# Kernel optimization log

Measured on AMD Instinct MI355X. Metric: run time of the kernel, lower is better.

The kernel has to match this reference:

```python
import jax, jax.numpy as jnp
import numpy as np
import hashlib

# Model hyperparameters (from VictorASIFractalLightModel defaults)
B, L, D = 2, 2048, 1024
VOCAB, TOOL_VOCAB = 65536, 128
STEPS = 8            # FractalEmbedding steps -> 2*STEPS = 16 features
N_CONV, N_ATTN = 10, 6
HEADS, Q_GROUPS = 8, 2
HPG = HEADS // Q_GROUPS
HEAD_DIM = D // HEADS
KSIZE = 5
EPS = 1e-5


def _token_to_c(token_ids_np):
    # sha256-based complex constant per token id (exactly as in FractalEmbedding)
    flat = token_ids_np.reshape(-1)
    out = np.empty((flat.size, 2), dtype=np.float32)
    for i, tid in enumerate(flat):
        h = hashlib.sha256(str(int(tid)).encode()).hexdigest()
        out[i, 0] = (int(h[:16], 16) / 2**64 - 0.5) * 2.0
        out[i, 1] = (int(h[16:32], 16) / 2**64 - 0.5) * 2.0
    return out.reshape(token_ids_np.shape + (2,))


def _julia_feats(cs):
    # Vectorized julia iteration, z starts at 0.  cs: [B, L, 2] -> feats [B, L, 2*STEPS]
    cr, ci = cs[..., 0], cs[..., 1]
    zr = jnp.zeros_like(cr)
    zi = jnp.zeros_like(ci)
    feats = []
    for _ in range(STEPS):
        zr, zi = zr * zr - zi * zi + cr, 2.0 * zr * zi + ci
        feats.append(zr)
        feats.append(zi)
    return jnp.stack(feats, axis=-1)


def _layer_norm(x, s, b):
    mu = jnp.mean(x, axis=-1, keepdims=True)
    var = jnp.mean(jnp.square(x - mu), axis=-1, keepdims=True)
    return (x - mu) * jax.lax.rsqrt(var + EPS) * s + b


def _conv_block(x, dw_w, dw_b, pw_w, pw_b, ln_s, ln_b):
    # x: [B, L, D] -> depthwise conv (k=5, same pad) -> pointwise conv to 2D -> GLU -> residual LN
    xc = jnp.transpose(x, (0, 2, 1))  # [B, D, L]
    y = jax.lax.conv_general_dilated(xc, dw_w, (1,), [(KSIZE // 2, KSIZE // 2)],
                                     dimension_numbers=("NCH", "OIH", "NCH"),
                                     feature_group_count=D) + dw_b[None, :, None]
    y = jax.lax.conv_general_dilated(y, pw_w, (1,), [(0, 0)],
                                     dimension_numbers=("NCH", "OIH", "NCH")) + pw_b[None, :, None]
    y = jnp.transpose(y, (0, 2, 1))  # [B, L, 2D]
    a, gate = jnp.split(y, 2, axis=-1)
    return _layer_norm(x + a * jax.nn.sigmoid(gate), ln_s, ln_b)


def _attention(x, qw, kvw, ow, ln_s, ln_b):
    # Grouped-query attention with an explicit (unfused) score tensor, per the source.
    Bx, Lx, Dx = x.shape
    q = (x @ qw).reshape(Bx, Lx, Q_GROUPS, HPG, HEAD_DIM)
    kv = (x @ kvw).reshape(Bx, Lx, HEADS, 2, HEAD_DIM)
    k = kv[..., 0, :].reshape(Bx, Lx, Q_GROUPS, HPG, HEAD_DIM)
    v = kv[..., 1, :].reshape(Bx, Lx, Q_GROUPS, HPG, HEAD_DIM)
    scale = HEAD_DIM ** -0.5
    scores = jnp.einsum("bqghd,bkghd->bghqk", q, k) * scale  # [B, g, hpg, Lq, Lk]
    attn = jax.nn.softmax(scores, axis=-1)
    out = jnp.einsum("bghqk,bkghd->bqghd", attn, v).reshape(Bx, Lx, Dx)
    return _layer_norm(x + out @ ow, ln_s, ln_b)


def setup_inputs() -> dict:
    key = jax.random.key(0)
    ks = jax.random.split(key, 10)
    token_ids = jax.random.randint(ks[0], (B, L), 0, VOCAB)
    cs = jnp.asarray(_token_to_c(np.asarray(token_ids)))
    return {
        "token_ids": token_ids,
        "cs": cs,
        "proj_w": jax.random.normal(ks[1], (2 * STEPS, D), dtype=jnp.float32) * 0.25,
        "emb_scale": jnp.ones((1,), dtype=jnp.float32),
        "conv_dw_w": jax.random.normal(ks[2], (N_CONV, D, 1, KSIZE), dtype=jnp.float32) * 0.2,
        "conv_dw_b": jnp.zeros((N_CONV, D), dtype=jnp.float32),
        "conv_pw_w": jax.random.normal(ks[3], (N_CONV, 2 * D, D, 1), dtype=jnp.float32) * (D ** -0.5),
        "conv_pw_b": jnp.zeros((N_CONV, 2 * D), dtype=jnp.float32),
        "conv_ln_s": jnp.ones((N_CONV, D), dtype=jnp.float32),
        "conv_ln_b": jnp.zeros((N_CONV, D), dtype=jnp.float32),
        "attn_q_w": jax.random.normal(ks[4], (N_ATTN, D, D), dtype=jnp.float32) * (D ** -0.5),
        "attn_kv_w": jax.random.normal(ks[5], (N_ATTN, D, 2 * D), dtype=jnp.float32) * (D ** -0.5),
        "attn_out_w": jax.random.normal(ks[6], (N_ATTN, D, D), dtype=jnp.float32) * (D ** -0.5),
        "attn_ln_s": jnp.ones((N_ATTN, D), dtype=jnp.float32),
        "attn_ln_b": jnp.zeros((N_ATTN, D), dtype=jnp.float32),
        "lm_w": jax.random.normal(ks[7], (D, VOCAB), dtype=jnp.float32) * (D ** -0.5),
        "tool_w": jax.random.normal(ks[8], (D, TOOL_VOCAB), dtype=jnp.float32) * (D ** -0.5),
        "tool_b": jnp.zeros((TOOL_VOCAB,), dtype=jnp.float32),
    }


def reference(token_ids, cs, proj_w, emb_scale, conv_dw_w, conv_dw_b, conv_pw_w, conv_pw_b,
              conv_ln_s, conv_ln_b, attn_q_w, attn_kv_w, attn_out_w, attn_ln_s, attn_ln_b,
              lm_w, tool_w, tool_b):
    feats = _julia_feats(cs)                 # [B, L, 16]
    h = (feats @ proj_w) * emb_scale         # FractalEmbedding
    for i in range(N_CONV):
        h = _conv_block(h, conv_dw_w[i], conv_dw_b[i], conv_pw_w[i], conv_pw_b[i],
                        conv_ln_s[i], conv_ln_b[i])
    for i in range(N_ATTN):
        h = _attention(h, attn_q_w[i], attn_kv_w[i], attn_out_w[i], attn_ln_s[i], attn_ln_b[i])
    # ReplayMemoryStack is a side-effecting identity on h.
    last = h[:, -1, :]
    gen_logits = last @ lm_w
    tool_logits = last @ tool_w + tool_b
    return gen_logits, tool_logits
```

## Files before the change

### kernel.cpp

```cpp
#include <hip/hip_runtime.h>
#include <hip/hip_bf16.h>
#include <math.h>

#define B_ 2
#define L_ 2048
#define D_ 1024
#define VOCAB_ 65536
#define TOOLV_ 128
#define NCONV_ 10
#define NATTN_ 6
#define HEADS_ 8
#define HD_ 128
#define EPS_ 1e-5f

typedef short bf16x8 __attribute__((ext_vector_type(8)));
typedef short short4v __attribute__((ext_vector_type(4)));
typedef float f32x4 __attribute__((ext_vector_type(4)));
#define MFMA16(a,b,c) __builtin_amdgcn_mfma_f32_16x16x32_bf16(a, b, c, 0, 0, 0)

__device__ inline short f2bf(float f) {
  __hip_bfloat16 h = __float2bfloat16(f);
  return *reinterpret_cast<short*>(&h);
}

__device__ __forceinline__ void gld16(const void* g, void* l) {
  __builtin_amdgcn_global_load_lds(
      (const __attribute__((address_space(1))) unsigned int*)g,
      (__attribute__((address_space(3))) unsigned int*)l, 16, 0, 0);
}

__device__ __forceinline__ void sync_prefetch() {
  asm volatile("s_waitcnt vmcnt(0)" ::: "memory");
  __builtin_amdgcn_s_barrier();
  __builtin_amdgcn_sched_barrier(0);
}

__global__ __launch_bounds__(256) void julia_proj_k(const float* __restrict__ cs,
    const float* __restrict__ pw, const float* __restrict__ esc, float* __restrict__ h) {
  int row = blockIdx.x;
  float cr = cs[2*(size_t)row], ci = cs[2*(size_t)row+1];
  float f[16];
  float zr = 0.f, zi = 0.f;
  #pragma unroll
  for (int s = 0; s < 8; ++s) {
    float nzr = zr*zr - zi*zi + cr;
    float nzi = 2.f*zr*zi + ci;
    zr = nzr; zi = nzi;
    f[2*s] = zr; f[2*s+1] = zi;
  }
  float e = esc[0];
  int d = threadIdx.x * 4;
  float4 acc = {0.f, 0.f, 0.f, 0.f};
  #pragma unroll
  for (int i = 0; i < 16; ++i) {
    float4 pv = *(const float4*)(pw + i*D_ + d);
    acc.x += f[i]*pv.x; acc.y += f[i]*pv.y; acc.z += f[i]*pv.z; acc.w += f[i]*pv.w;
  }
  acc.x *= e; acc.y *= e; acc.z *= e; acc.w *= e;
  *(float4*)(h + (size_t)row*D_ + d) = acc;
}

__global__ __launch_bounds__(256) void dwconv_k(const float* __restrict__ x,
    const float* __restrict__ w, const float* __restrict__ bias, short* __restrict__ y) {
  int idx = blockIdx.x*256 + threadIdx.x;
  int d = (idx & (D_/4 - 1)) * 4;
  int bl = idx >> 8;
  int l = bl & (L_-1);
  size_t bbase = (size_t)(bl >> 11) * L_;
  float4 acc = *(const float4*)(bias + d);
  float wr[4][5];
  #pragma unroll
  for (int j = 0; j < 4; ++j)
    #pragma unroll
    for (int k = 0; k < 5; ++k) wr[j][k] = w[(d+j)*5 + k];
  #pragma unroll
  for (int k = 0; k < 5; ++k) {
    int ll = l + k - 2;
    if (ll >= 0 && ll < L_) {
      float4 xv = *(const float4*)(x + (bbase + ll)*D_ + d);
      acc.x += xv.x*wr[0][k]; acc.y += xv.y*wr[1][k];
      acc.z += xv.z*wr[2][k]; acc.w += xv.w*wr[3][k];
    }
  }
  short4v o = { f2bf(acc.x), f2bf(acc.y), f2bf(acc.z), f2bf(acc.w) };
  ((short4v*)y)[idx] = o;
}

__global__ __launch_bounds__(256) void cvt_bf16_k(const float* __restrict__ x,
    short* __restrict__ y, int n4) {
  int i = blockIdx.x*256 + threadIdx.x;
  if (i >= n4) return;
  float4 v = ((const float4*)x)[i];
  short4v s = { f2bf(v.x), f2bf(v.y), f2bf(v.z), f2bf(v.w) };
  ((short4v*)y)[i] = s;
}

__global__ __launch_bounds__(256) void transp_bf16_k(const float* __restrict__ W0,
    short* __restrict__ WT0, int K, int N, size_t srcStride, size_t dstStride) {
  const float* W = W0 + blockIdx.z*srcStride;
  short* WT = WT0 + blockIdx.z*dstStride;
  __shared__ short t[32][33];
  int n0 = blockIdx.x*32, k0 = blockIdx.y*32;
  int tx = threadIdx.x & 31, ty = threadIdx.x >> 5;
  #pragma unroll
  for (int i = 0; i < 4; ++i) {
    int k = ty + i*8;
    t[tx][k] = f2bf(W[(size_t)(k0+k)*N + n0 + tx]);
  }
  __syncthreads();
  #pragma unroll
  for (int i = 0; i < 4; ++i) {
    int n = ty + i*8;
    WT[(size_t)(n0+n)*K + k0 + tx] = t[n][tx];
  }
}

template<int MODE, bool BIAS>
__global__ __launch_bounds__(256) void gemm_bf16(const short* __restrict__ A,
    const short* __restrict__ Bt, const float* __restrict__ bias,
    float* __restrict__ C, short* __restrict__ obf,
    short* __restrict__ kbf, short* __restrict__ vtbf,
    float scale, int M, int N, int K) {
  __shared__ short As[2][128*32];
  __shared__ short Bs[2][128*32];
  const int tid  = threadIdx.x;
  const int lane = tid & 63;
  const int wave = tid >> 6;
  const int wm = wave >> 1, wn = wave & 1;
  const int g = lane >> 4, c = lane & 15;
  const int m0 = blockIdx.x * 128, n0 = blockIdx.y * 128;

  f32x4 acc[4][4];
  #pragma unroll
  for (int i = 0; i < 4; ++i)
    #pragma unroll
    for (int j = 0; j < 4; ++j) acc[i][j] = (f32x4){0.f,0.f,0.f,0.f};

  const int srow = wave*16 + (lane>>2);
  const int scol = (lane&3)*8;
  const short* aSrc0 = A + (size_t)(m0 + srow)*K + scol;
  const short* aSrc1 = aSrc0 + (size_t)64*K;
  const short* bSrc0 = Bt + (size_t)(n0 + srow)*K + scol;
  const short* bSrc1 = bSrc0 + (size_t)64*K;
  const int woff = wave*512;

  gld16(aSrc0, &As[0][woff]);
  gld16(aSrc1, &As[0][woff + 2048]);
  gld16(bSrc0, &Bs[0][woff]);
  gld16(bSrc1, &Bs[0][woff + 2048]);
  sync_prefetch();

  const int nt = K >> 5;
  int cur = 0;
  for (int t = 0; t < nt; ++t) {
    if (t + 1 < nt) {
      int k0 = (t + 1) << 5;
      gld16(aSrc0 + k0, &As[cur^1][woff]);
      gld16(aSrc1 + k0, &As[cur^1][woff + 2048]);
      gld16(bSrc0 + k0, &Bs[cur^1][woff]);
      gld16(bSrc1 + k0, &Bs[cur^1][woff + 2048]);
    }
    bf16x8 af[4], bfr[4];
    #pragma unroll
    for (int mi = 0; mi < 4; ++mi)
      af[mi] = *(const bf16x8*)&As[cur][(wm*64 + mi*16 + c)*32 + g*8];
    #pragma unroll
    for (int ni = 0; ni < 4; ++ni)
      bfr[ni] = *(const bf16x8*)&Bs[cur][(wn*64 + ni*16 + c)*32 + g*8];
    #pragma unroll
    for (int mi = 0; mi < 4; ++mi)
      #pragma unroll
      for (int ni = 0; ni < 4; ++ni)
        acc[mi][ni] = MFMA16(af[mi], bfr[ni], acc[mi][ni]);
    if (t + 1 < nt) {
      sync_prefetch();
      cur ^= 1;
    }
  }

  #pragma unroll
  for (int mi = 0; mi < 4; ++mi) {
    int row = m0 + wm*64 + mi*16 + g*4;
    #pragma unroll
    for (int ni = 0; ni < 4; ++ni) {
      int col = n0 + wn*64 + ni*16 + c;
      if (MODE == 0) {
        float bv = BIAS ? bias[col] : 0.f;
        #pragma unroll
        for (int r = 0; r < 4; ++r)
          C[(size_t)(row+r)*N + col] = acc[mi][ni][r] + bv;
      } else {
        if (col < 1024) {
          #pragma unroll
          for (int r = 0; r < 4; ++r)
            obf[(size_t)(row+r)*1024 + col] = f2bf(acc[mi][ni][r]*scale);
        } else {
          int col2 = col - 1024;
          int hh = col2 >> 8, jj = (col2 >> 7) & 1, d = col2 & 127;
          int bb = row >> 11, l = row & 2047;
          size_t bh = (size_t)bb*8 + hh;
          if (jj == 0) {
            #pragma unroll
            for (int r = 0; r < 4; ++r)
              kbf[(bh*L_ + l + r)*128 + d] = f2bf(acc[mi][ni][r]);
          } else {
            #pragma unroll
            for (int r = 0; r < 4; ++r)
              vtbf[(bh*128 + d)*L_ + l + r] = f2bf(acc[mi][ni][r]);
          }
        }
      }
    }
  }
}

__global__ __launch_bounds__(256) void glu_ln_k(float* __restrict__ h,
    const float* __restrict__ y2, const float* __restrict__ s, const float* __restrict__ b,
    short* __restrict__ bo) {
  int row = blockIdx.x;
  int tid = threadIdx.x;
  int d = tid*4;
  float* xr = h + (size_t)row*D_;
  const float* yr = y2 + (size_t)row*2*D_;
  __shared__ float red[256];
  float4 xv = *(const float4*)(xr + d);
  float4 av = *(const float4*)(yr + d);
  float4 gv = *(const float4*)(yr + D_ + d);
  float v[4];
  v[0] = xv.x + av.x/(1.f + expf(-gv.x));
  v[1] = xv.y + av.y/(1.f + expf(-gv.y));
  v[2] = xv.z + av.z/(1.f + expf(-gv.z));
  v[3] = xv.w + av.w/(1.f + expf(-gv.w));
  red[tid] = v[0]+v[1]+v[2]+v[3]; __syncthreads();
  for (int st = 128; st > 0; st >>= 1) { if (tid < st) red[tid] += red[tid+st]; __syncthreads(); }
  float mu = red[0] * (1.f/D_); __syncthreads();
  float lv = 0.f;
  #pragma unroll
  for (int j = 0; j < 4; ++j) { float dd = v[j]-mu; lv += dd*dd; }
  red[tid] = lv; __syncthreads();
  for (int st = 128; st > 0; st >>= 1) { if (tid < st) red[tid] += red[tid+st]; __syncthreads(); }
  float var = red[0] * (1.f/D_);
  float r = 1.f/sqrtf(var + EPS_);
  float4 sv = *(const float4*)(s + d);
  float4 bv = *(const float4*)(b + d);
  float4 o;
  o.x = (v[0]-mu)*r*sv.x + bv.x;
  o.y = (v[1]-mu)*r*sv.y + bv.y;
  o.z = (v[2]-mu)*r*sv.z + bv.z;
  o.w = (v[3]-mu)*r*sv.w + bv.w;
  *(float4*)(xr + d) = o;
  if (bo) {
    short4v ob = { f2bf(o.x), f2bf(o.y), f2bf(o.z), f2bf(o.w) };
    *(short4v*)(bo + (size_t)row*D_ + d) = ob;
  }
}

__global__ __launch_bounds__(256) void resid_ln_k(float* __restrict__ h,
    const float* __restrict__ proj, const float* __restrict__ s, const float* __restrict__ b,
    short* __restrict__ bo) {
  int row = blockIdx.x;
  int tid = threadIdx.x;
  int d = tid*4;
  float* xr = h + (size_t)row*D_;
  const float* pr = proj + (size_t)row*D_;
  __shared__ float red[256];
  float4 xv = *(const float4*)(xr + d);
  float4 pv = *(const float4*)(pr + d);
  float v[4] = { xv.x+pv.x, xv.y+pv.y, xv.z+pv.z, xv.w+pv.w };
  red[tid] = v[0]+v[1]+v[2]+v[3]; __syncthreads();
  for (int st = 128; st > 0; st >>= 1) { if (tid < st) red[tid] += red[tid+st]; __syncthreads(); }
  float mu = red[0] * (1.f/D_); __syncthreads();
  float lv = 0.f;
  #pragma unroll
  for (int j = 0; j < 4; ++j) { float dd = v[j]-mu; lv += dd*dd; }
  red[tid] = lv; __syncthreads();
  for (int st = 128; st > 0; st >>= 1) { if (tid < st) red[tid] += red[tid+st]; __syncthreads(); }
  float var = red[0] * (1.f/D_);
  float r = 1.f/sqrtf(var + EPS_);
  float4 sv = *(const float4*)(s + d);
  float4 bv = *(const float4*)(b + d);
  float4 o;
  o.x = (v[0]-mu)*r*sv.x + bv.x;
  o.y = (v[1]-mu)*r*sv.y + bv.y;
  o.z = (v[2]-mu)*r*sv.z + bv.z;
  o.w = (v[3]-mu)*r*sv.w + bv.w;
  *(float4*)(xr + d) = o;
  if (bo) {
    short4v ob = { f2bf(o.x), f2bf(o.y), f2bf(o.z), f2bf(o.w) };
    *(short4v*)(bo + (size_t)row*D_ + d) = ob;
  }
}

#define PPITCH 72
__global__ __launch_bounds__(256) void attn2_k(const short* __restrict__ qbf,
    const short* __restrict__ kbf, const short* __restrict__ vtbf,
    short* __restrict__ obf) {
  __shared__ short Ks[2][64*128];
  __shared__ short Vts[2][128*64];
  __shared__ short Ps[4*16*PPITCH];

  const int tid  = threadIdx.x;
  const int wave = tid >> 6;
  const int lane = tid & 63;
  const int g    = lane >> 4;
  const int c    = lane & 15;
  const int hh   = blockIdx.y;
  const int b    = blockIdx.z;
  const int q0   = blockIdx.x*64 + wave*16;
  const size_t bh = (size_t)(b*HEADS_ + hh);

  bf16x8 qf[4];
  {
    const short* Qp = qbf + ((size_t)(b*L_ + q0 + c))*D_ + hh*HD_;
    #pragma unroll
    for (int kd = 0; kd < 4; ++kd)
      qf[kd] = *(const bf16x8*)(Qp + kd*32 + g*8);
  }

  f32x4 O[8];
  #pragma unroll
  for (int i = 0; i < 8; ++i) O[i] = (f32x4){0.f,0.f,0.f,0.f};
  float mrun[4] = {-INFINITY,-INFINITY,-INFINITY,-INFINITY};
  float lrun[4] = {0.f,0.f,0.f,0.f};
  short* Pw = Ps + wave*16*PPITCH;

  const short* kBase = kbf + bh*L_*128;
  const short* vBase = vtbf + bh*128*L_;

  auto stage = [&](int t, int buf) {
    #pragma unroll
    for (int rd = 0; rd < 4; ++rd) {
      int slot = rd*256 + tid;
      int kr = slot >> 4, kj = slot & 15;
      int vr = slot >> 3, vj = slot & 7;
      gld16(kBase + ((size_t)(t*64 + kr))*128 + ((kj ^ (kr & 15)) * 8),
            (char*)&Ks[buf][0] + (rd*256 + wave*64)*16);
      gld16(vBase + (size_t)vr*L_ + t*64 + ((vj ^ (vr & 7)) * 8),
            (char*)&Vts[buf][0] + (rd*256 + wave*64)*16);
    }
  };

  stage(0, 0);
  sync_prefetch();
  int cur = 0;
  const int NT = L_/64;

  for (int t = 0; t < NT; ++t) {
    if (t + 1 < NT) stage(t + 1, cur^1);

    f32x4 s[4];
    #pragma unroll
    for (int nc = 0; nc < 4; ++nc) {
      s[nc] = (f32x4){0.f,0.f,0.f,0.f};
      int R = nc*16 + c;
      #pragma unroll
      for (int kd = 0; kd < 4; ++kd) {
        bf16x8 kf = *(const bf16x8*)&Ks[cur][R*128 + (((kd*4 + g) ^ (R & 15)) * 8)];
        s[nc] = MFMA16(qf[kd], kf, s[nc]);
      }
    }

    float tm[4], rsum[4], alpha[4];
    #pragma unroll
    for (int r = 0; r < 4; ++r)
      tm[r] = fmaxf(fmaxf(s[0][r], s[1][r]), fmaxf(s[2][r], s[3][r]));
    #pragma unroll
    for (int r = 0; r < 4; ++r) {
      #pragma unroll
      for (int mask = 1; mask <= 8; mask <<= 1)
        tm[r] = fmaxf(tm[r], __shfl_xor(tm[r], mask));
      float mnew = fmaxf(mrun[r], tm[r]);
      alpha[r] = expf(mrun[r] - mnew);
      mrun[r] = mnew;
      rsum[r] = 0.f;
    }
    #pragma unroll
    for (int nc = 0; nc < 4; ++nc)
      #pragma unroll
      for (int r = 0; r < 4; ++r) {
        float p = expf(s[nc][r] - mrun[r]);
        s[nc][r] = p;
        rsum[r] += p;
      }
    #pragma unroll
    for (int r = 0; r < 4; ++r) {
      #pragma unroll
      for (int mask = 1; mask <= 8; mask <<= 1)
        rsum[r] += __shfl_xor(rsum[r], mask);
      lrun[r] = lrun[r]*alpha[r] + rsum[r];
    }
    #pragma unroll
    for (int nc = 0; nc < 8; ++nc)
      #pragma unroll
      for (int r = 0; r < 4; ++r) O[nc][r] *= alpha[r];

    #pragma unroll
    for (int nc = 0; nc < 4; ++nc)
      #pragma unroll
      for (int r = 0; r < 4; ++r)
        Pw[(g*4+r)*PPITCH + nc*16 + c] = f2bf(s[nc][r]);
    asm volatile("s_waitcnt lgkmcnt(0)" ::: "memory");
    bf16x8 pa0 = *(const bf16x8*)&Pw[c*PPITCH + g*8];
    bf16x8 pa1 = *(const bf16x8*)&Pw[c*PPITCH + 32 + g*8];

    #pragma unroll
    for (int ks = 0; ks < 2; ++ks) {
      #pragma unroll
      for (int nc = 0; nc < 8; ++nc) {
        int R = nc*16 + c;
        bf16x8 vf = *(const bf16x8*)&Vts[cur][R*64 + (((ks*4 + g) ^ (R & 7)) * 8)];
        O[nc] = MFMA16(ks ? pa1 : pa0, vf, O[nc]);
      }
    }

    if (t + 1 < NT) {
      sync_prefetch();
      cur ^= 1;
    }
  }

  short* ob = obf + ((size_t)(b*L_ + q0))*D_ + hh*HD_;
  #pragma unroll
  for (int r = 0; r < 4; ++r) {
    float inv = 1.f / lrun[r];
    #pragma unroll
    for (int nc = 0; nc < 8; ++nc)
      ob[(size_t)(g*4+r)*D_ + nc*16 + c] = f2bf(O[nc][r] * inv);
  }
}

__global__ __launch_bounds__(256) void lm_head_part_k(const float* __restrict__ h,
    const float* __restrict__ lm_w, float* __restrict__ part) {
  int tid = threadIdx.x;
  int n = (blockIdx.x*256 + tid)*4;
  int ks = blockIdx.y;
  __shared__ float last0[256], last1[256];
  const float* h0 = h + ((size_t)0*L_ + (L_-1))*D_ + ks*256;
  const float* h1 = h + ((size_t)1*L_ + (L_-1))*D_ + ks*256;
  last0[tid] = h0[tid]; last1[tid] = h1[tid];
  __syncthreads();
  float4 a0 = {0.f,0.f,0.f,0.f}, a1 = {0.f,0.f,0.f,0.f};
  const float* wp = lm_w + (size_t)(ks*256)*VOCAB_ + n;
  for (int kk = 0; kk < 256; ++kk) {
    float4 wv = *(const float4*)(wp + (size_t)kk*VOCAB_);
    float c0 = last0[kk], c1 = last1[kk];
    a0.x += c0*wv.x; a0.y += c0*wv.y; a0.z += c0*wv.z; a0.w += c0*wv.w;
    a1.x += c1*wv.x; a1.y += c1*wv.y; a1.z += c1*wv.z; a1.w += c1*wv.w;
  }
  *(float4*)(part + ((size_t)ks*2 + 0)*VOCAB_ + n) = a0;
  *(float4*)(part + ((size_t)ks*2 + 1)*VOCAB_ + n) = a1;
}

__global__ __launch_bounds__(256) void lm_head_red_k(const float* __restrict__ part,
    float* __restrict__ out) {
  int i = blockIdx.x*256 + threadIdx.x;
  int j = (i*4) / VOCAB_;
  int n = (i*4) & (VOCAB_-1);
  float4 acc = {0.f,0.f,0.f,0.f};
  #pragma unroll
  for (int ks = 0; ks < 4; ++ks) {
    float4 v = *(const float4*)(part + ((size_t)ks*2 + j)*VOCAB_ + n);
    acc.x += v.x; acc.y += v.y; acc.z += v.z; acc.w += v.w;
  }
  *(float4*)(out + (size_t)j*VOCAB_ + n) = acc;
}

__global__ __launch_bounds__(128) void tool_head_k(const float* __restrict__ h,
    const float* __restrict__ tw, const float* __restrict__ tb, float* __restrict__ out) {
  int b = blockIdx.x;
  int tid = threadIdx.x;
  __shared__ float last[D_];
  const float* hr = h + ((size_t)b*L_ + (L_-1))*D_;
  for (int d = tid; d < D_; d += 128) last[d] = hr[d];
  __syncthreads();
  float acc = tb[tid];
  for (int k = 0; k < D_; ++k) acc += last[k]*tw[(size_t)k*TOOLV_ + tid];
  out[(size_t)2*VOCAB_ + (size_t)b*TOOLV_ + tid] = acc;
}

extern "C" void kernel_launch(void* const* d_in, const int* in_sizes, int n_in,
                              void* d_out, int out_size, void* d_ws, size_t ws_size,
                              hipStream_t stream) {
  const float* cs        = (const float*)d_in[1];
  const float* proj_w    = (const float*)d_in[2];
  const float* emb_scale = (const float*)d_in[3];
  const float* conv_dw_w = (const float*)d_in[4];
  const float* conv_dw_b = (const float*)d_in[5];
  const float* conv_pw_w = (const float*)d_in[6];
  const float* conv_pw_b = (const float*)d_in[7];
  const float* conv_ln_s = (const float*)d_in[8];
  const float* conv_ln_b = (const float*)d_in[9];
  const float* attn_q_w  = (const float*)d_in[10];
  const float* attn_kv_w = (const float*)d_in[11];
  const float* attn_out_w= (const float*)d_in[12];
  const float* attn_ln_s = (const float*)d_in[13];
  const float* attn_ln_b = (const float*)d_in[14];
  const float* lm_w      = (const float*)d_in[15];
  const float* tool_w    = (const float*)d_in[16];
  const float* tool_b    = (const float*)d_in[17];

  const int M = B_*L_;
  float* h    = (float*)d_ws;
  float* buf2 = h    + (size_t)M*D_;
  short* kbf  = (short*)(buf2 + (size_t)M*2*D_);
  short* vtbf = kbf + (size_t)B_*HEADS_*L_*128;
  short* abf  = (short*)(vtbf + (size_t)B_*HEADS_*128*L_);
  short* wconv= abf + (size_t)M*D_;
  short* wqkv = wconv + (size_t)NCONV_*2*D_*D_;
  short* wout = wqkv + (size_t)NATTN_*3*D_*D_;
  float* lmpart = (float*)(wout + (size_t)NATTN_*D_*D_);
  short* qbf  = (short*)(buf2 + (size_t)M*D_);

  const float scale = 0.088388347648318447f;

  {
    int n4 = NCONV_*2*D_*D_/4;
    cvt_bf16_k<<<(n4 + 255)/256, 256, 0, stream>>>(conv_pw_w, wconv, n4);
    transp_bf16_k<<<dim3(D_/32, D_/32, NATTN_), 256, 0, stream>>>(
        attn_q_w, wqkv, D_, D_, (size_t)D_*D_, (size_t)3*D_*D_);
    transp_bf16_k<<<dim3((2*D_)/32, D_/32, NATTN_), 256, 0, stream>>>(
        attn_kv_w, wqkv + (size_t)D_*D_, D_, 2*D_, (size_t)D_*2*D_, (size_t)3*D_*D_);
    transp_bf16_k<<<dim3(D_/32, D_/32, NATTN_), 256, 0, stream>>>(
        attn_out_w, wout, D_, D_, (size_t)D_*D_, (size_t)D_*D_);
  }

  julia_proj_k<<<M, 256, 0, stream>>>(cs, proj_w, emb_scale, h);

  for (int i = 0; i < NCONV_; ++i) {
    dwconv_k<<<(M*D_/4)/256, 256, 0, stream>>>(h, conv_dw_w + (size_t)i*D_*5,
                                               conv_dw_b + (size_t)i*D_, abf);
    gemm_bf16<0, true><<<dim3(M/128, (2*D_)/128), 256, 0, stream>>>(
        abf, wconv + (size_t)i*2*D_*D_, conv_pw_b + (size_t)i*2*D_,
        buf2, nullptr, nullptr, nullptr, 1.f, M, 2*D_, D_);
    glu_ln_k<<<M, 256, 0, stream>>>(h, buf2, conv_ln_s + (size_t)i*D_,
                                    conv_ln_b + (size_t)i*D_,
                                    (i == NCONV_-1) ? abf : (short*)nullptr);
  }

  for (int i = 0; i < NATTN_; ++i) {
    gemm_bf16<3, false><<<dim3(M/128, (3*D_)/128), 256, 0, stream>>>(
        abf, wqkv + (size_t)i*3*D_*D_, nullptr, nullptr, qbf, kbf, vtbf,
        scale, M, 3*D_, D_);
    attn2_k<<<dim3(L_/64, HEADS_, B_), 256, 0, stream>>>(qbf, kbf, vtbf, abf);
    gemm_bf16<0, false><<<dim3(M/128, D_/128), 256, 0, stream>>>(
        abf, wout + (size_t)i*D_*D_, nullptr, buf2, nullptr, nullptr, nullptr,
        1.f, M, D_, D_);
    resid_ln_k<<<M, 256, 0, stream>>>(h, buf2, attn_ln_s + (size_t)i*D_,
                                      attn_ln_b + (size_t)i*D_,
                                      (i < NATTN_-1) ? abf : (short*)nullptr);
  }

  lm_head_part_k<<<dim3(VOCAB_/1024, 4), 256, 0, stream>>>(h, lm_w, lmpart);
  lm_head_red_k<<<(2*VOCAB_/4)/256, 256, 0, stream>>>(lmpart, (float*)d_out);
  tool_head_k<<<B_, 128, 0, stream>>>(h, tool_w, tool_b, (float*)d_out);
}
```

Before: 1.811 ms.

## Fuse GLU into pointwise GEMM epilogue and swizzle GEMM/attention block order

The conv pointwise weights are row-permuted at setup so that each GEMM tile holds matching 'a' and 'gate' columns. The GEMM epilogue can then apply bias and sigmoid gating and write a single D-wide output, and the LayerNorm reuses the plain residual kernel. This removes writing and re-reading the 2D-wide intermediate. Workgroup IDs in the GEMM and attention kernels are also remapped with a stride-8 swizzle, probably to spread blocks across XCDs and improve L2 locality. The swizzle hardcodes grid sizes (32 M-tiles, a 512-block attention grid), which ties the kernels to these shapes.

```diff
diff --git a/kernel.cpp b/kernel.cpp
--- a/kernel.cpp
+++ b/kernel.cpp
@@ -86,13 +86,19 @@
   ((short4v*)y)[idx] = o;
 }
 
-__global__ __launch_bounds__(256) void cvt_bf16_k(const float* __restrict__ x,
-    short* __restrict__ y, int n4) {
-  int i = blockIdx.x*256 + threadIdx.x;
-  if (i >= n4) return;
-  float4 v = ((const float4*)x)[i];
+__global__ __launch_bounds__(256) void cvt_perm_k(const float* __restrict__ W,
+    short* __restrict__ out) {
+  int z = blockIdx.y;
+  int i4 = blockIdx.x*256 + threadIdx.x;
+  int e = i4*4;
+  int r = e >> 10, k = e & 1023;
+  int t = r >> 7, wn = (r >> 6) & 1, j = r & 63;
+  int u = t*64 + wn*32 + (j & 31);
+  int src = (j < 32) ? u : 1024 + u;
+  const float* p = W + ((size_t)z*2048 + src)*1024 + k;
+  float4 v = *(const float4*)p;
   short4v s = { f2bf(v.x), f2bf(v.y), f2bf(v.z), f2bf(v.w) };
-  ((short4v*)y)[i] = s;
+  *(short4v*)(out + ((size_t)z*2048 + r)*1024 + k) = s;
 }
 
 __global__ __launch_bounds__(256) void transp_bf16_k(const float* __restrict__ W0,
@@ -115,7 +121,7 @@
   }
 }
 
-template<int MODE, bool BIAS>
+template<int MODE>
 __global__ __launch_bounds__(256) void gemm_bf16(const short* __restrict__ A,
     const short* __restrict__ Bt, const float* __restrict__ bias,
     float* __restrict__ C, short* __restrict__ obf,
@@ -128,7 +134,12 @@
   const int wave = tid >> 6;
   const int wm = wave >> 1, wn = wave & 1;
   const int g = lane >> 4, c = lane & 15;
-  const int m0 = blockIdx.x * 128, n0 = blockIdx.y * 128;
+
+  int flat = blockIdx.y * gridDim.x + blockIdx.x;
+  int nwg  = gridDim.x * gridDim.y;
+  int swz  = (flat & 7) * (nwg >> 3) + (flat >> 3);
+  const int m0 = (swz & 31) * 128;
+  const int n0 = (swz >> 5) * 128;
 
   f32x4 acc[4][4];
   #pragma unroll
@@ -178,6 +189,25 @@
     }
   }
 
+  if (MODE == 4) {
+    #pragma unroll
+    for (int mi = 0; mi < 4; ++mi) {
+      int row = m0 + wm*64 + mi*16 + g*4;
+      #pragma unroll
+      for (int ni = 0; ni < 2; ++ni) {
+        int u = (n0 >> 7)*64 + wn*32 + ni*16 + c;
+        float ba = bias[u], bg = bias[1024 + u];
+        #pragma unroll
+        for (int r = 0; r < 4; ++r) {
+          float a  = acc[mi][ni][r]   + ba;
+          float gt = acc[mi][ni+2][r] + bg;
+          C[(size_t)(row+r)*1024 + u] = a / (1.f + expf(-gt));
+        }
+      }
+    }
+    return;
+  }
+
   #pragma unroll
   for (int mi = 0; mi < 4; ++mi) {
     int row = m0 + wm*64 + mi*16 + g*4;
@@ -185,10 +215,9 @@
     for (int ni = 0; ni < 4; ++ni) {
       int col = n0 + wn*64 + ni*16 + c;
       if (MODE == 0) {
-        float bv = BIAS ? bias[col] : 0.f;
         #pragma unroll
         for (int r = 0; r < 4; ++r)
-          C[(size_t)(row+r)*N + col] = acc[mi][ni][r] + bv;
+          C[(size_t)(row+r)*N + col] = acc[mi][ni][r];
       } else {
         if (col < 1024) {
           #pragma unroll
@@ -214,23 +243,18 @@
   }
 }
 
-__global__ __launch_bounds__(256) void glu_ln_k(float* __restrict__ h,
-    const float* __restrict__ y2, const float* __restrict__ s, const float* __restrict__ b,
+__global__ __launch_bounds__(256) void resid_ln_k(float* __restrict__ h,
+    const float* __restrict__ proj, const float* __restrict__ s, const float* __restrict__ b,
     short* __restrict__ bo) {
   int row = blockIdx.x;
   int tid = threadIdx.x;
   int d = tid*4;
   float* xr = h + (size_t)row*D_;
-  const float* yr = y2 + (size_t)row*2*D_;
+  const float* pr = proj + (size_t)row*D_;
   __shared__ float red[256];
   float4 xv = *(const float4*)(xr + d);
-  float4 av = *(const float4*)(yr + d);
-  float4 gv = *(const float4*)(yr + D_ + d);
-  float v[4];
-  v[0] = xv.x + av.x/(1.f + expf(-gv.x));
-  v[1] = xv.y + av.y/(1.f + expf(-gv.y));
-  v[2] = xv.z + av.z/(1.f + expf(-gv.z));
-  v[3] = xv.w + av.w/(1.f + expf(-gv.w));
+  float4 pv = *(const float4*)(pr + d);
+  float v[4] = { xv.x+pv.x, xv.y+pv.y, xv.z+pv.z, xv.w+pv.w };
   red[tid] = v[0]+v[1]+v[2]+v[3]; __syncthreads();
   for (int st = 128; st > 0; st >>= 1) { if (tid < st) red[tid] += red[tid+st]; __syncthreads(); }
   float mu = red[0] * (1.f/D_); __syncthreads();
@@ -255,42 +279,6 @@
   }
 }
 
-__global__ __launch_bounds__(256) void resid_ln_k(float* __restrict__ h,
-    const float* __restrict__ proj, const float* __restrict__ s, const float* __restrict__ b,
-    short* __restrict__ bo) {
-  int row = blockIdx.x;
-  int tid = threadIdx.x;
-  int d = tid*4;
-  float* xr = h + (size_t)row*D_;
-  const float* pr = proj + (size_t)row*D_;
-  __shared__ float red[256];
-  float4 xv = *(const float4*)(xr + d);
-  float4 pv = *(const float4*)(pr + d);
-  float v[4] = { xv.x+pv.x, xv.y+pv.y, xv.z+pv.z, xv.w+pv.w };
-  red[tid] = v[0]+v[1]+v[2]+v[3]; __syncthreads();
-  for (int st = 128; st > 0; st >>= 1) { if (tid < st) red[tid] += red[tid+st]; __syncthreads(); }
-  float mu = red[0] * (1.f/D_); __syncthreads();
-  float lv = 0.f;
-  #pragma unroll
-  for (int j = 0; j < 4; ++j) { float dd = v[j]-mu; lv += dd*dd; }
-  red[tid] = lv; __syncthreads();
-  for (int st = 128; st > 0; st >>= 1) { if (tid < st) red[tid] += red[tid+st]; __syncthreads(); }
-  float var = red[0] * (1.f/D_);
-  float r = 1.f/sqrtf(var + EPS_);
-  float4 sv = *(const float4*)(s + d);
-  float4 bv = *(const float4*)(b + d);
-  float4 o;
-  o.x = (v[0]-mu)*r*sv.x + bv.x;
-  o.y = (v[1]-mu)*r*sv.y + bv.y;
-  o.z = (v[2]-mu)*r*sv.z + bv.z;
-  o.w = (v[3]-mu)*r*sv.w + bv.w;
-  *(float4*)(xr + d) = o;
-  if (bo) {
-    short4v ob = { f2bf(o.x), f2bf(o.y), f2bf(o.z), f2bf(o.w) };
-    *(short4v*)(bo + (size_t)row*D_ + d) = ob;
-  }
-}
-
 #define PPITCH 72
 __global__ __launch_bounds__(256) void attn2_k(const short* __restrict__ qbf,
     const short* __restrict__ kbf, const short* __restrict__ vtbf,
@@ -304,9 +292,13 @@
   const int lane = tid & 63;
   const int g    = lane >> 4;
   const int c    = lane & 15;
-  const int hh   = blockIdx.y;
-  const int b    = blockIdx.z;
-  const int q0   = blockIdx.x*64 + wave*16;
+
+  int flat = blockIdx.x;
+  int swz  = (flat & 7)*64 + (flat >> 3);
+  const int qt = swz & 31;
+  const int hh = (swz >> 5) & 7;
+  const int b  = swz >> 8;
+  const int q0 = qt*64 + wave*16;
   const size_t bh = (size_t)(b*HEADS_ + hh);
 
   bf16x8 qf[4];
@@ -514,8 +506,7 @@
   const float scale = 0.088388347648318447f;
 
   {
-    int n4 = NCONV_*2*D_*D_/4;
-    cvt_bf16_k<<<(n4 + 255)/256, 256, 0, stream>>>(conv_pw_w, wconv, n4);
+    cvt_perm_k<<<dim3((2*D_*D_/4)/256, NCONV_), 256, 0, stream>>>(conv_pw_w, wconv);
     transp_bf16_k<<<dim3(D_/32, D_/32, NATTN_), 256, 0, stream>>>(
         attn_q_w, wqkv, D_, D_, (size_t)D_*D_, (size_t)3*D_*D_);
     transp_bf16_k<<<dim3((2*D_)/32, D_/32, NATTN_), 256, 0, stream>>>(
@@ -529,20 +520,20 @@
   for (int i = 0; i < NCONV_; ++i) {
     dwconv_k<<<(M*D_/4)/256, 256, 0, stream>>>(h, conv_dw_w + (size_t)i*D_*5,
                                                conv_dw_b + (size_t)i*D_, abf);
-    gemm_bf16<0, true><<<dim3(M/128, (2*D_)/128), 256, 0, stream>>>(
+    gemm_bf16<4><<<dim3(M/128, (2*D_)/128), 256, 0, stream>>>(
         abf, wconv + (size_t)i*2*D_*D_, conv_pw_b + (size_t)i*2*D_,
         buf2, nullptr, nullptr, nullptr, 1.f, M, 2*D_, D_);
-    glu_ln_k<<<M, 256, 0, stream>>>(h, buf2, conv_ln_s + (size_t)i*D_,
-                                    conv_ln_b + (size_t)i*D_,
-                                    (i == NCONV_-1) ? abf : (short*)nullptr);
+    resid_ln_k<<<M, 256, 0, stream>>>(h, buf2, conv_ln_s + (size_t)i*D_,
+                                      conv_ln_b + (size_t)i*D_,
+                                      (i == NCONV_-1) ? abf : (short*)nullptr);
   }
 
   for (int i = 0; i < NATTN_; ++i) {
-    gemm_bf16<3, false><<<dim3(M/128, (3*D_)/128), 256, 0, stream>>>(
+    gemm_bf16<3><<<dim3(M/128, (3*D_)/128), 256, 0, stream>>>(
         abf, wqkv + (size_t)i*3*D_*D_, nullptr, nullptr, qbf, kbf, vtbf,
         scale, M, 3*D_, D_);
-    attn2_k<<<dim3(L_/64, HEADS_, B_), 256, 0, stream>>>(qbf, kbf, vtbf, abf);
-    gemm_bf16<0, false><<<dim3(M/128, D_/128), 256, 0, stream>>>(
+    attn2_k<<<(L_/64)*HEADS_*B_, 256, 0, stream>>>(qbf, kbf, vtbf, abf);
+    gemm_bf16<0><<<dim3(M/128, D_/128), 256, 0, stream>>>(
         abf, wout + (size_t)i*D_*D_, nullptr, buf2, nullptr, nullptr, nullptr,
         1.f, M, D_, D_);
     resid_ln_k<<<M, 256, 0, stream>>>(h, buf2, attn_ln_s + (size_t)i*D_,
```

New measurement: 1.801 ms. About the same (-0.6%).
